# Optimization experiments

Hardware: AMD Instinct MI355X
Metric: run time of the kernel (lower is better)

Reference implementation:

```python
import jax, jax.numpy as jnp
import numpy as np

B = 2          # batch size
G = 96         # voxel grid extent per dim
RES = 0.04     # voxel resolution (meters)
STRIDE = 1.0   # sparse tensor stride
EPS = 1e-5     # batchnorm eps
C_SP = 32      # sparse feature channels
C_PF = 32      # pts_feat channels
H = 128        # hidden conv channels
NHYP = 7       # 2h+1, h=3


def setup_inputs():
    key = jax.random.key(0)
    ks = jax.random.split(key, 16)
    n = 150_000
    N = 2 * 9 * 56 * 56  # b * n_views * 56x56
    sparse_coords = jax.random.randint(ks[0], (n, 3), 0, G, dtype=jnp.int32)
    sparse_batch = jnp.sort(jax.random.randint(ks[1], (n,), 0, B, dtype=jnp.int32))
    sparse_feats = jax.random.normal(ks[2], (n, C_SP), jnp.float32)
    sparse_pts = sparse_coords.astype(jnp.float32) * RES  # world coordinates
    pts_depthmap_hyp = jax.random.uniform(ks[3], (N, NHYP, 3), jnp.float32) * (0.9 * G * RES)
    pts_feat = jax.random.normal(ks[4], (N, NHYP, C_PF), jnp.float32)
    pts_batch = jax.random.randint(ks[5], (N,), 0, B, dtype=jnp.int32)
    c_in = C_SP + C_PF
    def cw(k, o, i):
        return jax.random.normal(k, (o, i, 3), jnp.float32) * (1.0 / np.sqrt(i * 3))
    inp = dict(sparse_pts=sparse_pts, sparse_coords=sparse_coords, sparse_batch=sparse_batch,
               sparse_feats=sparse_feats, pts_depthmap_hyp=pts_depthmap_hyp,
               pts_feat=pts_feat, pts_batch=pts_batch)
    for li, (o, i, kk) in enumerate([(H, c_in, ks[6]), (H, H, ks[7]), (H, H, ks[8])], start=1):
        kw, km = jax.random.split(kk)
        inp[f'w{li}'] = cw(kw, o, i)
        inp[f'g{li}'] = jnp.ones((o,), jnp.float32)
        inp[f'b{li}'] = jnp.zeros((o,), jnp.float32)
        inp[f'm{li}'] = jax.random.normal(km, (o,), jnp.float32) * 0.1
        inp[f'v{li}'] = jnp.ones((o,), jnp.float32)
    inp['w4'] = cw(ks[9], 1, H)
    inp['bias4'] = jnp.zeros((1,), jnp.float32)
    return inp


def _trilinear_interp(coords, cbatch, feats, q, qb):
    """Sparse trilinear interpolation (MinkowskiInterpolation, stride 1).
    coords:(n,3) int voxel coords, cbatch:(n,), feats:(n,c), q:(M,3) float, qb:(M,).
    Missing corner voxels contribute zero."""
    n = coords.shape[0]
    keys = ((cbatch * G + coords[:, 0]) * G + coords[:, 1]) * G + coords[:, 2]
    order = jnp.argsort(keys)
    skeys = keys[order]
    sfeats = feats[order]
    fl = jnp.floor(q)
    frac = q - fl
    fli = fl.astype(jnp.int32)
    out = jnp.zeros((q.shape[0], feats.shape[1]), feats.dtype)
    for dx in (0, 1):
        for dy in (0, 1):
            for dz in (0, 1):
                c = fli + jnp.array([dx, dy, dz], jnp.int32)
                w = ((frac[:, 0] if dx else 1.0 - frac[:, 0]) *
                     (frac[:, 1] if dy else 1.0 - frac[:, 1]) *
                     (frac[:, 2] if dz else 1.0 - frac[:, 2]))
                qkey = ((qb * G + c[:, 0]) * G + c[:, 1]) * G + c[:, 2]
                idx = jnp.clip(jnp.searchsorted(skeys, qkey), 0, n - 1)
                hit = (skeys[idx] == qkey) & jnp.all((c >= 0) & (c < G), axis=1)
                out = out + jnp.where(hit, w, 0.0)[:, None] * sfeats[idx]
    return out


def _conv1d(x, w):  # x:(N,C,L), w:(O,C,3), pad 1
    return jax.lax.conv_general_dilated(x, w, (1,), [(1, 1)],
                                        dimension_numbers=('NCH', 'OIH', 'NCH'))


def _bn_relu(x, g, b, m, v):
    s = (g / jnp.sqrt(v + EPS))[None, :, None]
    return jax.nn.relu((x - m[None, :, None]) * s + b[None, :, None])


def reference(sparse_pts, sparse_coords, sparse_batch, sparse_feats,
              pts_depthmap_hyp, pts_feat, pts_batch,
              w1, g1, b1, m1, v1, w2, g2, b2, m2, v2, w3, g3, b3, m3, v3, w4, bias4):
    N, n_hyp = pts_depthmap_hyp.shape[0], pts_depthmap_hyp.shape[1]
    # scatter-min of point coordinates per batch element
    min_pts = jax.ops.segment_min(sparse_pts, sparse_batch, num_segments=B)  # (B,3)
    pts_idx = (pts_depthmap_hyp - min_pts[pts_batch][:, None, :]) / RES * STRIDE
    q = pts_idx.reshape(N * n_hyp, 3)
    qb = jnp.repeat(pts_batch, n_hyp)
    feats = _trilinear_interp(sparse_coords, sparse_batch, sparse_feats, q, qb)
    feats = feats.reshape(N, n_hyp, -1)
    x = jnp.concatenate([feats, pts_feat], axis=2).transpose(0, 2, 1)  # (N, C, n_hyp)
    h = _bn_relu(_conv1d(x, w1), g1, b1, m1, v1)
    h = _bn_relu(_conv1d(h, w2), g2, b2, m2, v2)
    h = _bn_relu(_conv1d(h, w3), g3, b3, m3, v3)
    logits = _conv1d(h, w4) + bias4[None, :, None]  # (N,1,n_hyp)
    return jax.nn.softmax(logits[:, 0, :], axis=1)  # (N, n_hyp)
```

## Files before the change

kernel.cpp:

```cpp
#include <hip/hip_runtime.h>

#define GG 96
#define NB 2
#define RESV 0.04f

constexpr int NG  = NB * GG * GG * GG;
constexpr int PT  = 16;
constexpr int NCOLS = PT * 8;
constexpr int XC  = NCOLS + 2;
constexpr int CS  = 136;

typedef _Float16 f16x8 __attribute__((ext_vector_type(8)));
typedef _Float16 f16x4 __attribute__((ext_vector_type(4)));
typedef _Float16 f16x2 __attribute__((ext_vector_type(2)));
typedef float    f32x4 __attribute__((ext_vector_type(4)));

__global__ void k_init(int4* __restrict__ grid4, int* __restrict__ minc) {
    int i = blockIdx.x * 256 + threadIdx.x;
    if (i < NG / 4) grid4[i] = make_int4(0x7fffffff, 0x7fffffff, 0x7fffffff, 0x7fffffff);
    if (i < 6)      minc[i] = 0x7fffffff;
}

__global__ void k_scatter(const int* __restrict__ coords, const int* __restrict__ sbatch,
                          int n, int* __restrict__ grid, int* __restrict__ minc) {
    __shared__ int lmin[6];
    int tid = threadIdx.x;
    if (tid < 6) lmin[tid] = 0x7fffffff;
    __syncthreads();
    int i = blockIdx.x * 256 + tid;
    if (i < n) {
        int cx = coords[3*i], cy = coords[3*i+1], cz = coords[3*i+2];
        int b = sbatch[i];
        atomicMin(&grid[((b*GG + cx)*GG + cy)*GG + cz], i);
        atomicMin(&lmin[b*3+0], cx);
        atomicMin(&lmin[b*3+1], cy);
        atomicMin(&lmin[b*3+2], cz);
    }
    __syncthreads();
    if (tid < 6) atomicMin(&minc[tid], lmin[tid]);
}

__global__ void k_wconv(const float* __restrict__ w1, const float* __restrict__ w2,
                        const float* __restrict__ w3,
                        const float* __restrict__ g1, const float* __restrict__ b1,
                        const float* __restrict__ m1, const float* __restrict__ v1,
                        const float* __restrict__ g2, const float* __restrict__ b2,
                        const float* __restrict__ m2, const float* __restrict__ v2,
                        const float* __restrict__ g3, const float* __restrict__ b3,
                        const float* __restrict__ m3, const float* __restrict__ v3,
                        _Float16* __restrict__ o1, _Float16* __restrict__ o2,
                        _Float16* __restrict__ o3, float* __restrict__ tvec) {
    int e = blockIdx.x * 256 + threadIdx.x;
    if (e < 24576) {
        int j = e & 7, lane = (e >> 3) & 63, t2 = e >> 9;
        int mt = t2 / 6, ks = t2 % 6;
        int row = mt * 16 + (lane & 15);
        int k = ks * 32 + ((lane >> 4) << 3) + j;
        int tap = k >> 6, c = k & 63;
        float s = g1[row] / sqrtf(v1[row] + 1e-5f);
        o1[e] = (_Float16)(w1[(row * 64 + c) * 3 + tap] * s);
    } else if (e < 122880) {
        int u = e - 24576;
        int layer = u / 49152;
        u %= 49152;
        int j = u & 7, lane = (u >> 3) & 63, t2 = u >> 9;
        int mt = t2 / 12, ks = t2 % 12;
        int row = mt * 16 + (lane & 15);
        int k = ks * 32 + ((lane >> 4) << 3) + j;
        int tap = k >> 7, c = k & 127;
        const float* w = layer ? w3 : w2;
        const float* g = layer ? g3 : g2;
        const float* v = layer ? v3 : v2;
        float s = g[row] / sqrtf(v[row] + 1e-5f);
        (layer ? o3 : o2)[u] = (_Float16)(w[(row * 128 + c) * 3 + tap] * s);
    } else if (e < 123264) {
        int i = e - 122880;
        int layer = i >> 7, ch = i & 127;
        const float* g = layer == 0 ? g1 : (layer == 1 ? g2 : g3);
        const float* b = layer == 0 ? b1 : (layer == 1 ? b2 : b3);
        const float* m = layer == 0 ? m1 : (layer == 1 ? m2 : m3);
        const float* v = layer == 0 ? v1 : (layer == 1 ? v2 : v3);
        float s = g[ch] / sqrtf(v[ch] + 1e-5f);
        tvec[i] = b[ch] - m[ch] * s;
    }
}

template<int CIN, int KS>
__device__ __forceinline__ void conv_layer(
    const _Float16* xin, const _Float16* __restrict__ wg,
    const float* tvl, _Float16* hout, int tid)
{
    const int wave = tid >> 6;
    const int lane = tid & 63;
    const int quad = lane >> 4;
    const int l15  = lane & 15;
    const int mp   = wave & 1;
    const int cb   = (wave >> 1) * 64;

    constexpr int PF = 3;
    f32x4 acc[4][4] = {};
    f16x8 Abuf[PF][4];
    f16x8 Bbuf[2][4];

    const _Float16* wbase = wg + (((size_t)(mp * 4) * KS) * 64 + lane) * 8;

    auto loadA = [&](int slot, int ks) {
#pragma unroll
        for (int m = 0; m < 4; ++m)
            Abuf[slot][m] = *(const f16x8*)(wbase + (size_t)(m * KS + ks) * 512);
    };
    auto loadB = [&](int slot, int ks) {
        const int k0   = ks * 32 + quad * 8;
        const int tap  = k0 / CIN;
        const int c    = k0 & (CIN - 1);
        const int boff = (cb + l15 + tap) * CS + c;
#pragma unroll
        for (int ct = 0; ct < 4; ++ct)
            Bbuf[slot][ct] = *(const f16x8*)(xin + boff + ct * 16 * CS);
    };

#pragma unroll
    for (int p = 0; p < PF; ++p) loadA(p, p);
    loadB(0, 0);

#pragma unroll
    for (int ks = 0; ks < KS; ++ks) {
        if (ks + 1 < KS) loadB((ks + 1) & 1, ks + 1);
#pragma unroll
        for (int ct = 0; ct < 4; ++ct)
#pragma unroll
            for (int m = 0; m < 4; ++m)
                acc[ct][m] = __builtin_amdgcn_mfma_f32_16x16x32_f16(
                    Abuf[ks % PF][m], Bbuf[ks & 1][ct], acc[ct][m], 0, 0, 0);
        if (ks + PF < KS) loadA(ks % PF, ks + PF);
    }

    if ((l15 & 7) != 7) {
#pragma unroll
        for (int ct = 0; ct < 4; ++ct) {
            const int outc = cb + ct * 16 + l15;
            _Float16* dst = hout + (outc + 1) * CS + mp * 64 + quad * 4;
#pragma unroll
            for (int m = 0; m < 4; ++m) {
                const int ch = mp * 64 + m * 16 + quad * 4;
                f32x4 tval = *(const f32x4*)(tvl + ch);
                f16x4 o;
#pragma unroll
                for (int i = 0; i < 4; ++i)
                    o[i] = (_Float16)fmaxf(acc[ct][m][i] + tval[i], 0.f);
                *(f16x4*)(dst + m * 16) = o;
            }
        }
    }
}

__global__ __launch_bounds__(256, 2) void k_main(
    const float* __restrict__ pdh, const float* __restrict__ ptsfeat,
    const int* __restrict__ pts_batch, const float* __restrict__ sfeats,
    const int* __restrict__ grid, const int* __restrict__ minc,
    const _Float16* __restrict__ w16_1, const _Float16* __restrict__ w16_2,
    const _Float16* __restrict__ w16_3, const float* __restrict__ tvec,
    const float* __restrict__ w4, const float* __restrict__ bias4,
    float* __restrict__ out, int N, int n_sp)
{
    __shared__ __align__(16) _Float16 hA[XC * CS];
    __shared__ __align__(16) _Float16 hB[XC * CS];
    __shared__ __align__(16) float    tv[384];
    __shared__ __align__(16) _Float16 w4h[384];
    __shared__ float lg[NCOLS];

    const int tid = threadIdx.x;
    const int p0  = blockIdx.x * PT;

    for (int e = tid; e < 384; e += 256) {
        tv[e]  = tvec[e];
        w4h[e] = (_Float16)w4[(e & 127) * 3 + (e >> 7)];
    }
    for (int idx = tid; idx < 18 * (CS / 2); idx += 256) {
        int cidx = idx / (CS / 2), off = idx % (CS / 2);
        int u = (cidx < 17) ? cidx * 8 : 129;
        ((int*)hA)[u * (CS / 2) + off] = 0;
        ((int*)hB)[u * (CS / 2) + off] = 0;
    }

    if (tid < 224) {
        int q = tid >> 1, part = tid & 1;
        int pl = q / 7, j = q - pl * 7;
        int pg = p0 + pl;
        if (pg < N) {
            const f32x4* pf = (const f32x4*)(ptsfeat + ((size_t)pg * 7 + j) * 32 + part * 16);
            f32x4 pf0 = __builtin_nontemporal_load(pf + 0);
            f32x4 pf1 = __builtin_nontemporal_load(pf + 1);
            f32x4 pf2 = __builtin_nontemporal_load(pf + 2);
            f32x4 pf3 = __builtin_nontemporal_load(pf + 3);
            const float* pd = pdh + ((size_t)pg * 7 + j) * 3;
            float px = pd[0], py = pd[1], pz = pd[2];
            int b = pts_batch[pg];
            int mA0 = minc[0], mA1 = minc[1], mA2 = minc[2];
            int mB0 = minc[3], mB1 = minc[4], mB2 = minc[5];
            int m0 = b ? mB0 : mA0;
            int m1 = b ? mB1 : mA1;
            int m2 = b ? mB2 : mA2;
            float qx = (px - (float)m0 * RESV) / RESV;
            float qy = (py - (float)m1 * RESV) / RESV;
            float qz = (pz - (float)m2 * RESV) / RESV;
            float flx = floorf(qx), fly = floorf(qy), flz = floorf(qz);
            float fx = qx - flx, fy = qy - fly, fz = qz - flz;
            int ix0 = (int)flx, iy0 = (int)fly, iz0 = (int)flz;
            const int gbase = b * (GG * GG * GG);

            int   si[8];
            float wc[8];
#pragma unroll
            for (int c = 0; c < 8; ++c) {
                int dx = c >> 2, dy = (c >> 1) & 1, dz = c & 1;
                int cx = ix0 + dx, cy = iy0 + dy, cz = iz0 + dz;
                bool ok = ((unsigned)cx < GG) & ((unsigned)cy < GG) & ((unsigned)cz < GG);
                int cell = gbase + (cx * GG + cy) * GG + cz;
                wc[c] = ok ? (dx ? fx : 1.f - fx) * (dy ? fy : 1.f - fy)
                             * (dz ? fz : 1.f - fz)
                           : 0.f;
                si[c] = grid[ok ? cell : 0];
            }
            const f32x4* fb = (const f32x4*)sfeats;
            const f32x4* fpc[8];
            float w8[8];
#pragma unroll
            for (int c = 0; c < 8; ++c) {
                bool hit = si[c] < n_sp;
                w8[c]  = hit ? wc[c] : 0.f;
                fpc[c] = fb + (size_t)(hit ? si[c] : 0) * 8 + part * 4;
            }
            float acc[16];
#pragma unroll
            for (int k2 = 0; k2 < 16; ++k2) acc[k2] = 0.f;
#pragma unroll
            for (int c = 0; c < 8; ++c) {
                f32x4 f0 = fpc[c][0], f1 = fpc[c][1], f2 = fpc[c][2], f3 = fpc[c][3];
                float w = w8[c];
#pragma unroll
                for (int k2 = 0; k2 < 4; ++k2) {
                    acc[k2]      += w * f0[k2];
                    acc[4 + k2]  += w * f1[k2];
                    acc[8 + k2]  += w * f2[k2];
                    acc[12 + k2] += w * f3[k2];
                }
            }
            int u = pl * 8 + 1 + j;
            _Float16* xp = hA + u * CS + part * 16;
            f16x8 h0, h1;
#pragma unroll
            for (int k2 = 0; k2 < 8; ++k2) { h0[k2] = (_Float16)acc[k2]; h1[k2] = (_Float16)acc[8 + k2]; }
            *(f16x8*)xp = h0;
            *(f16x8*)(xp + 8) = h1;
            f16x8 p0v, p1v;
#pragma unroll
            for (int k2 = 0; k2 < 4; ++k2) {
                p0v[k2]     = (_Float16)pf0[k2];
                p0v[4 + k2] = (_Float16)pf1[k2];
                p1v[k2]     = (_Float16)pf2[k2];
                p1v[4 + k2] = (_Float16)pf3[k2];
            }
            *(f16x8*)(hA + u * CS + 32 + part * 16) = p0v;
            *(f16x8*)(hA + u * CS + 40 + part * 16) = p1v;
        }
    }
    __syncthreads();

    conv_layer<64,  6>(hA, w16_1, tv,       hB, tid);
    __syncthreads();
    conv_layer<128, 12>(hB, w16_2, tv + 128, hA, tid);
    __syncthreads();
    conv_layer<128, 12>(hA, w16_3, tv + 256, hB, tid);
    __syncthreads();

    {
        int col = tid >> 1, part = tid & 1;
        float sum = 0.f;
        if ((col & 7) != 7) {
#pragma unroll
            for (int t = 0; t < 3; ++t) {
                const _Float16* hp = hB + (col + t) * CS;
                const _Float16* wr = w4h + t * 128;
#pragma unroll
                for (int c8 = 0; c8 < 8; ++c8) {
                    int chunk = 2 * c8 + part;
                    f16x8 h8 = *(const f16x8*)(hp + chunk * 8);
                    f16x8 w8 = *(const f16x8*)(wr + chunk * 8);
#pragma unroll
                    for (int p = 0; p < 4; ++p) {
                        f16x2 hv = { h8[2*p], h8[2*p+1] };
                        f16x2 wv = { w8[2*p], w8[2*p+1] };
#if __has_builtin(__builtin_amdgcn_fdot2)
                        sum = __builtin_amdgcn_fdot2(hv, wv, sum, false);
#else
                        sum += (float)hv[0]*(float)wv[0] + (float)hv[1]*(float)wv[1];
#endif
                    }
                }
            }
        }
        sum += __shfl_xor(sum, 1);
        if (part == 0 && (col & 7) != 7) lg[col] = sum + bias4[0];
    }
    __syncthreads();

    if (tid < PT) {
        int pg = p0 + tid;
        if (pg < N) {
            float l0[7];
            float mx = -1e30f;
#pragma unroll
            for (int j = 0; j < 7; ++j) { l0[j] = lg[tid * 8 + j]; mx = fmaxf(mx, l0[j]); }
            float s = 0.f;
#pragma unroll
            for (int j = 0; j < 7; ++j) { l0[j] = __expf(l0[j] - mx); s += l0[j]; }
            float inv = 1.f / s;
#pragma unroll
            for (int j = 0; j < 7; ++j) out[(size_t)pg * 7 + j] = l0[j] * inv;
        }
    }
}

extern "C" void kernel_launch(void* const* d_in, const int* in_sizes, int n_in,
                              void* d_out, int out_size, void* d_ws, size_t ws_size,
                              hipStream_t stream) {
    const int*   sparse_coords = (const int*)d_in[1];
    const int*   sparse_batch  = (const int*)d_in[2];
    const float* sparse_feats  = (const float*)d_in[3];
    const float* pdh           = (const float*)d_in[4];
    const float* ptsfeat       = (const float*)d_in[5];
    const int*   pts_batch     = (const int*)d_in[6];
    const float* w1 = (const float*)d_in[7];
    const float* g1 = (const float*)d_in[8],  *b1 = (const float*)d_in[9];
    const float* m1 = (const float*)d_in[10], *v1 = (const float*)d_in[11];
    const float* w2 = (const float*)d_in[12];
    const float* g2 = (const float*)d_in[13], *b2 = (const float*)d_in[14];
    const float* m2 = (const float*)d_in[15], *v2 = (const float*)d_in[16];
    const float* w3 = (const float*)d_in[17];
    const float* g3 = (const float*)d_in[18], *b3 = (const float*)d_in[19];
    const float* m3 = (const float*)d_in[20], *v3 = (const float*)d_in[21];
    const float* w4 = (const float*)d_in[22];
    const float* bias4 = (const float*)d_in[23];

    const int n_sp = in_sizes[2];
    const int N    = in_sizes[6];

    int* grid = (int*)d_ws;
    int* minc = grid + NG;
    _Float16* w16_1 = (_Float16*)((char*)d_ws + (size_t)(NG + 6) * 4 + 8);
    _Float16* w16_2 = w16_1 + 128 * 192;
    _Float16* w16_3 = w16_2 + 128 * 384;
    float*    tvec  = (float*)(w16_3 + 128 * 384);

    k_init<<<(NG / 4 + 255) / 256, 256, 0, stream>>>((int4*)grid, minc);
    k_scatter<<<(n_sp + 255) / 256, 256, 0, stream>>>(sparse_coords, sparse_batch,
                                                      n_sp, grid, minc);
    k_wconv<<<482, 256, 0, stream>>>(w1, w2, w3,
                                     g1, b1, m1, v1, g2, b2, m2, v2, g3, b3, m3, v3,
                                     w16_1, w16_2, w16_3, tvec);
    k_main<<<(N + PT - 1) / PT, 256, 0, stream>>>(
        pdh, ptsfeat, pts_batch, sparse_feats, grid, minc,
        w16_1, w16_2, w16_3, tvec, w4, bias4, (float*)d_out, N, n_sp);
}
```

Measured before the change: 158.1 us.

## Make main kernel persistent and software-pipeline the gather across conv layers

The main kernel becomes persistent: a grid of at most 512 blocks loops over point tiles. The gather and interpolation for the next tile is split into stages (global loads, grid lookups, feature accumulation, LDS write) placed between the three conv layers of the current tile, so memory latency overlaps MFMA work. The shared-memory logit buffer and its extra barrier are replaced by a wave-shuffle softmax. In exchange, register pressure rises from the live prefetch state, and load balance depends on the fixed grid size.

```diff
diff --git a/kernel.cpp b/kernel.cpp
--- a/kernel.cpp
+++ b/kernel.cpp
@@ -167,10 +167,10 @@
     __shared__ __align__(16) _Float16 hB[XC * CS];
     __shared__ __align__(16) float    tv[384];
     __shared__ __align__(16) _Float16 w4h[384];
-    __shared__ float lg[NCOLS];
 
     const int tid = threadIdx.x;
-    const int p0  = blockIdx.x * PT;
+    const int G   = gridDim.x;
+    const int ntiles = (N + PT - 1) / PT;
 
     for (int e = tid; e < 384; e += 256) {
         tv[e]  = tvec[e];
@@ -178,39 +178,63 @@
     }
     for (int idx = tid; idx < 18 * (CS / 2); idx += 256) {
         int cidx = idx / (CS / 2), off = idx % (CS / 2);
-        int u = (cidx < 17) ? cidx * 8 : 129;
-        ((int*)hA)[u * (CS / 2) + off] = 0;
-        ((int*)hB)[u * (CS / 2) + off] = 0;
-    }
-
-    if (tid < 224) {
-        int q = tid >> 1, part = tid & 1;
-        int pl = q / 7, j = q - pl * 7;
-        int pg = p0 + pl;
-        if (pg < N) {
-            const f32x4* pf = (const f32x4*)(ptsfeat + ((size_t)pg * 7 + j) * 32 + part * 16);
-            f32x4 pf0 = __builtin_nontemporal_load(pf + 0);
-            f32x4 pf1 = __builtin_nontemporal_load(pf + 1);
-            f32x4 pf2 = __builtin_nontemporal_load(pf + 2);
-            f32x4 pf3 = __builtin_nontemporal_load(pf + 3);
-            const float* pd = pdh + ((size_t)pg * 7 + j) * 3;
-            float px = pd[0], py = pd[1], pz = pd[2];
-            int b = pts_batch[pg];
-            int mA0 = minc[0], mA1 = minc[1], mA2 = minc[2];
-            int mB0 = minc[3], mB1 = minc[4], mB2 = minc[5];
-            int m0 = b ? mB0 : mA0;
-            int m1 = b ? mB1 : mA1;
-            int m2 = b ? mB2 : mA2;
+        int u2 = (cidx < 17) ? cidx * 8 : 129;
+        ((int*)hA)[u2 * (CS / 2) + off] = 0;
+        ((int*)hB)[u2 * (CS / 2) + off] = 0;
+    }
+
+    const bool ip  = tid < 224;
+    const int  q   = tid >> 1, part = tid & 1;
+    const int  pl  = q / 7, jj = q - pl * 7;
+    const int  u   = pl * 8 + 1 + jj;
+    const int  mA0 = minc[0], mA1 = minc[1], mA2 = minc[2];
+    const int  mB0 = minc[3], mB1 = minc[4], mB2 = minc[5];
+    const float b4 = bias4[0];
+
+    f32x4 pf0, pf1, pf2, pf3;
+    float px = 0.f, py = 0.f, pz = 0.f;
+    int   bsel = 0;
+    int   si[8];
+    float wc[8];
+    f16x8 p0v, p1v, h0, h1;
+    bool  nv = false;
+
+    auto stage1 = [&](int tt) {
+        nv = false;
+        if (ip && tt < ntiles) {
+            int pg = tt * PT + pl;
+            if (pg < N) {
+                nv = true;
+                const f32x4* pf = (const f32x4*)(ptsfeat + ((size_t)pg * 7 + jj) * 32 + part * 16);
+                pf0 = __builtin_nontemporal_load(pf + 0);
+                pf1 = __builtin_nontemporal_load(pf + 1);
+                pf2 = __builtin_nontemporal_load(pf + 2);
+                pf3 = __builtin_nontemporal_load(pf + 3);
+                const float* pd = pdh + ((size_t)pg * 7 + jj) * 3;
+                px = pd[0]; py = pd[1]; pz = pd[2];
+                bsel = pts_batch[pg];
+            }
+        }
+    };
+    auto stage2 = [&]() {
+        if (nv) {
+#pragma unroll
+            for (int k2 = 0; k2 < 4; ++k2) {
+                p0v[k2]     = (_Float16)pf0[k2];
+                p0v[4 + k2] = (_Float16)pf1[k2];
+                p1v[k2]     = (_Float16)pf2[k2];
+                p1v[4 + k2] = (_Float16)pf3[k2];
+            }
+            int m0 = bsel ? mB0 : mA0;
+            int m1 = bsel ? mB1 : mA1;
+            int m2 = bsel ? mB2 : mA2;
             float qx = (px - (float)m0 * RESV) / RESV;
             float qy = (py - (float)m1 * RESV) / RESV;
             float qz = (pz - (float)m2 * RESV) / RESV;
             float flx = floorf(qx), fly = floorf(qy), flz = floorf(qz);
             float fx = qx - flx, fy = qy - fly, fz = qz - flz;
             int ix0 = (int)flx, iy0 = (int)fly, iz0 = (int)flz;
-            const int gbase = b * (GG * GG * GG);
-
-            int   si[8];
-            float wc[8];
+            const int gbase = bsel * (GG * GG * GG);
 #pragma unroll
             for (int c = 0; c < 8; ++c) {
                 int dx = c >> 2, dy = (c >> 1) & 1, dz = c & 1;
@@ -222,6 +246,10 @@
                            : 0.f;
                 si[c] = grid[ok ? cell : 0];
             }
+        }
+    };
+    auto stage3 = [&]() {
+        if (nv) {
             const f32x4* fb = (const f32x4*)sfeats;
             const f32x4* fpc[8];
             float w8[8];
@@ -246,79 +274,82 @@
                     acc[12 + k2] += w * f3[k2];
                 }
             }
-            int u = pl * 8 + 1 + j;
+#pragma unroll
+            for (int k2 = 0; k2 < 8; ++k2) {
+                h0[k2] = (_Float16)acc[k2];
+                h1[k2] = (_Float16)acc[8 + k2];
+            }
+        }
+    };
+    auto writeR = [&]() {
+        if (nv) {
             _Float16* xp = hA + u * CS + part * 16;
-            f16x8 h0, h1;
-#pragma unroll
-            for (int k2 = 0; k2 < 8; ++k2) { h0[k2] = (_Float16)acc[k2]; h1[k2] = (_Float16)acc[8 + k2]; }
-            *(f16x8*)xp = h0;
+            *(f16x8*)xp       = h0;
             *(f16x8*)(xp + 8) = h1;
-            f16x8 p0v, p1v;
-#pragma unroll
-            for (int k2 = 0; k2 < 4; ++k2) {
-                p0v[k2]     = (_Float16)pf0[k2];
-                p0v[4 + k2] = (_Float16)pf1[k2];
-                p1v[k2]     = (_Float16)pf2[k2];
-                p1v[4 + k2] = (_Float16)pf3[k2];
-            }
             *(f16x8*)(hA + u * CS + 32 + part * 16) = p0v;
             *(f16x8*)(hA + u * CS + 40 + part * 16) = p1v;
         }
-    }
+    };
+
+    int tile = blockIdx.x;
+    stage1(tile); stage2(); stage3(); writeR();
     __syncthreads();
 
-    conv_layer<64,  6>(hA, w16_1, tv,       hB, tid);
-    __syncthreads();
-    conv_layer<128, 12>(hB, w16_2, tv + 128, hA, tid);
-    __syncthreads();
-    conv_layer<128, 12>(hA, w16_3, tv + 256, hB, tid);
-    __syncthreads();
-
-    {
-        int col = tid >> 1, part = tid & 1;
-        float sum = 0.f;
-        if ((col & 7) != 7) {
-#pragma unroll
-            for (int t = 0; t < 3; ++t) {
-                const _Float16* hp = hB + (col + t) * CS;
-                const _Float16* wr = w4h + t * 128;
-#pragma unroll
-                for (int c8 = 0; c8 < 8; ++c8) {
-                    int chunk = 2 * c8 + part;
-                    f16x8 h8 = *(const f16x8*)(hp + chunk * 8);
-                    f16x8 w8 = *(const f16x8*)(wr + chunk * 8);
-#pragma unroll
-                    for (int p = 0; p < 4; ++p) {
-                        f16x2 hv = { h8[2*p], h8[2*p+1] };
-                        f16x2 wv = { w8[2*p], w8[2*p+1] };
+    for (; tile < ntiles; tile += G) {
+        stage1(tile + G);
+        conv_layer<64,  6>(hA, w16_1, tv,       hB, tid);
+        __syncthreads();
+        stage2();
+        conv_layer<128, 12>(hB, w16_2, tv + 128, hA, tid);
+        __syncthreads();
+        stage3();
+        conv_layer<128, 12>(hA, w16_3, tv + 256, hB, tid);
+        __syncthreads();
+        writeR();
+        {
+            int col = tid >> 1, p4 = tid & 1;
+            float sum = 0.f;
+            if ((col & 7) != 7) {
+#pragma unroll
+                for (int t = 0; t < 3; ++t) {
+                    const _Float16* hp = hB + (col + t) * CS;
+                    const _Float16* wr = w4h + t * 128;
+#pragma unroll
+                    for (int c8 = 0; c8 < 8; ++c8) {
+                        int chunk = 2 * c8 + p4;
+                        f16x8 h8 = *(const f16x8*)(hp + chunk * 8);
+                        f16x8 w8 = *(const f16x8*)(wr + chunk * 8);
+#pragma unroll
+                        for (int p = 0; p < 4; ++p) {
+                            f16x2 hv = { h8[2*p], h8[2*p+1] };
+                            f16x2 wv = { w8[2*p], w8[2*p+1] };
 #if __has_builtin(__builtin_amdgcn_fdot2)
-                        sum = __builtin_amdgcn_fdot2(hv, wv, sum, false);
+                            sum = __builtin_amdgcn_fdot2(hv, wv, sum, false);
 #else
-                        sum += (float)hv[0]*(float)wv[0] + (float)hv[1]*(float)wv[1];
+                            sum += (float)hv[0]*(float)wv[0] + (float)hv[1]*(float)wv[1];
 #endif
+                        }
                     }
                 }
             }
-        }
-        sum += __shfl_xor(sum, 1);
-        if (part == 0 && (col & 7) != 7) lg[col] = sum + bias4[0];
-    }
-    __syncthreads();
-
-    if (tid < PT) {
-        int pg = p0 + tid;
-        if (pg < N) {
-            float l0[7];
-            float mx = -1e30f;
-#pragma unroll
-            for (int j = 0; j < 7; ++j) { l0[j] = lg[tid * 8 + j]; mx = fmaxf(mx, l0[j]); }
-            float s = 0.f;
-#pragma unroll
-            for (int j = 0; j < 7; ++j) { l0[j] = __expf(l0[j] - mx); s += l0[j]; }
-            float inv = 1.f / s;
-#pragma unroll
-            for (int j = 0; j < 7; ++j) out[(size_t)pg * 7 + j] = l0[j] * inv;
-        }
+            sum += __shfl_xor(sum, 1);
+            float logit = sum + b4;
+            bool  dead  = (col & 7) == 7;
+            float v = dead ? -1e30f : logit;
+            v = fmaxf(v, __shfl_xor(v, 2));
+            v = fmaxf(v, __shfl_xor(v, 4));
+            v = fmaxf(v, __shfl_xor(v, 8));
+            float e = (!dead && p4 == 0) ? __expf(logit - v) : 0.f;
+            float es = e;
+            es += __shfl_xor(es, 2);
+            es += __shfl_xor(es, 4);
+            es += __shfl_xor(es, 8);
+            if (p4 == 0 && !dead) {
+                int pgt = tile * PT + (col >> 3);
+                if (pgt < N) out[(size_t)pgt * 7 + (col & 7)] = e / es;
+            }
+        }
+        __syncthreads();
     }
 }
 
@@ -359,7 +390,9 @@
     k_wconv<<<482, 256, 0, stream>>>(w1, w2, w3,
                                      g1, b1, m1, v1, g2, b2, m2, v2, g3, b3, m3, v3,
                                      w16_1, w16_2, w16_3, tvec);
-    k_main<<<(N + PT - 1) / PT, 256, 0, stream>>>(
+    const int ntiles = (N + PT - 1) / PT;
+    const int gsz = ntiles < 512 ? ntiles : 512;
+    k_main<<<gsz, 256, 0, stream>>>(
         pdh, ptsfeat, pts_batch, sparse_feats, grid, minc,
         w16_1, w16_2, w16_3, tvec, w4, bias4, (float*)d_out, N, n_sp);
 }
```

After: 436.5 us. 2.76x slower.

## Split trilinear interpolation into separate kernel and shuffle-based softmax

Applied to the files above, without the earlier changes.

Moves the gather-heavy trilinear interpolation and pts_feat conversion out of the conv kernel into a standalone high-occupancy kernel that writes fp16 inputs to a global workspace buffer. The main kernel then just copies these inputs into LDS, so its latency-bound gathers no longer stall the MFMA-heavy block. The softmax now uses warp shuffles instead of an LDS round trip and an extra barrier. The cost is an extra global write and read of about 56k*7*64 fp16 values, plus one more kernel launch.

```diff
diff --git a/kernel.cpp b/kernel.cpp
--- a/kernel.cpp
+++ b/kernel.cpp
@@ -85,6 +85,92 @@
     }
 }
 
+__global__ __launch_bounds__(256, 4) void k_interp(
+    const float* __restrict__ pdh, const float* __restrict__ ptsfeat,
+    const int* __restrict__ pts_batch, const float* __restrict__ sfeats,
+    const int* __restrict__ grid, const int* __restrict__ minc,
+    _Float16* __restrict__ Xg, int NQ, int n_sp)
+{
+    int t = blockIdx.x * 256 + threadIdx.x;
+    int gq = t >> 1, part = t & 1;
+    if (gq >= NQ) return;
+    int pg = gq / 7;
+
+    const f32x4* pf = (const f32x4*)(ptsfeat + (size_t)gq * 32 + part * 16);
+    f32x4 pf0 = __builtin_nontemporal_load(pf + 0);
+    f32x4 pf1 = __builtin_nontemporal_load(pf + 1);
+    f32x4 pf2 = __builtin_nontemporal_load(pf + 2);
+    f32x4 pf3 = __builtin_nontemporal_load(pf + 3);
+    const float* pd = pdh + (size_t)gq * 3;
+    float px = pd[0], py = pd[1], pz = pd[2];
+    int b = pts_batch[pg];
+    int mA0 = minc[0], mA1 = minc[1], mA2 = minc[2];
+    int mB0 = minc[3], mB1 = minc[4], mB2 = minc[5];
+    int m0 = b ? mB0 : mA0;
+    int m1 = b ? mB1 : mA1;
+    int m2 = b ? mB2 : mA2;
+    float qx = (px - (float)m0 * RESV) / RESV;
+    float qy = (py - (float)m1 * RESV) / RESV;
+    float qz = (pz - (float)m2 * RESV) / RESV;
+    float flx = floorf(qx), fly = floorf(qy), flz = floorf(qz);
+    float fx = qx - flx, fy = qy - fly, fz = qz - flz;
+    int ix0 = (int)flx, iy0 = (int)fly, iz0 = (int)flz;
+    const int gbase = b * (GG * GG * GG);
+
+    int   si[8];
+    float wc[8];
+#pragma unroll
+    for (int c = 0; c < 8; ++c) {
+        int dx = c >> 2, dy = (c >> 1) & 1, dz = c & 1;
+        int cx = ix0 + dx, cy = iy0 + dy, cz = iz0 + dz;
+        bool ok = ((unsigned)cx < GG) & ((unsigned)cy < GG) & ((unsigned)cz < GG);
+        int cell = gbase + (cx * GG + cy) * GG + cz;
+        wc[c] = ok ? (dx ? fx : 1.f - fx) * (dy ? fy : 1.f - fy)
+                     * (dz ? fz : 1.f - fz)
+                   : 0.f;
+        si[c] = grid[ok ? cell : 0];
+    }
+    const f32x4* fb = (const f32x4*)sfeats;
+    const f32x4* fpc[8];
+    float w8[8];
+#pragma unroll
+    for (int c = 0; c < 8; ++c) {
+        bool hit = si[c] < n_sp;
+        w8[c]  = hit ? wc[c] : 0.f;
+        fpc[c] = fb + (size_t)(hit ? si[c] : 0) * 8 + part * 4;
+    }
+    float acc[16];
+#pragma unroll
+    for (int k2 = 0; k2 < 16; ++k2) acc[k2] = 0.f;
+#pragma unroll
+    for (int c = 0; c < 8; ++c) {
+        f32x4 f0 = fpc[c][0], f1 = fpc[c][1], f2 = fpc[c][2], f3 = fpc[c][3];
+        float w = w8[c];
+#pragma unroll
+        for (int k2 = 0; k2 < 4; ++k2) {
+            acc[k2]      += w * f0[k2];
+            acc[4 + k2]  += w * f1[k2];
+            acc[8 + k2]  += w * f2[k2];
+            acc[12 + k2] += w * f3[k2];
+        }
+    }
+    f16x8 h0, h1, p0v, p1v;
+#pragma unroll
+    for (int k2 = 0; k2 < 8; ++k2) { h0[k2] = (_Float16)acc[k2]; h1[k2] = (_Float16)acc[8 + k2]; }
+#pragma unroll
+    for (int k2 = 0; k2 < 4; ++k2) {
+        p0v[k2]     = (_Float16)pf0[k2];
+        p0v[4 + k2] = (_Float16)pf1[k2];
+        p1v[k2]     = (_Float16)pf2[k2];
+        p1v[4 + k2] = (_Float16)pf3[k2];
+    }
+    _Float16* xp = Xg + (size_t)gq * 64;
+    *(f16x8*)(xp + part * 16)          = h0;
+    *(f16x8*)(xp + part * 16 + 8)      = h1;
+    *(f16x8*)(xp + 32 + part * 16)     = p0v;
+    *(f16x8*)(xp + 32 + part * 16 + 8) = p1v;
+}
+
 template<int CIN, int KS>
 __device__ __forceinline__ void conv_layer(
     const _Float16* xin, const _Float16* __restrict__ wg,
@@ -155,19 +241,16 @@
 }
 
 __global__ __launch_bounds__(256, 2) void k_main(
-    const float* __restrict__ pdh, const float* __restrict__ ptsfeat,
-    const int* __restrict__ pts_batch, const float* __restrict__ sfeats,
-    const int* __restrict__ grid, const int* __restrict__ minc,
+    const _Float16* __restrict__ Xg,
     const _Float16* __restrict__ w16_1, const _Float16* __restrict__ w16_2,
     const _Float16* __restrict__ w16_3, const float* __restrict__ tvec,
     const float* __restrict__ w4, const float* __restrict__ bias4,
-    float* __restrict__ out, int N, int n_sp)
+    float* __restrict__ out, int N)
 {
     __shared__ __align__(16) _Float16 hA[XC * CS];
     __shared__ __align__(16) _Float16 hB[XC * CS];
     __shared__ __align__(16) float    tv[384];
     __shared__ __align__(16) _Float16 w4h[384];
-    __shared__ float lg[NCOLS];
 
     const int tid = threadIdx.x;
     const int p0  = blockIdx.x * PT;
@@ -184,85 +267,18 @@
     }
 
     if (tid < 224) {
-        int q = tid >> 1, part = tid & 1;
-        int pl = q / 7, j = q - pl * 7;
+        int qi = tid >> 1, part = tid & 1;
+        int pl = qi / 7, j = qi - pl * 7;
         int pg = p0 + pl;
         if (pg < N) {
-            const f32x4* pf = (const f32x4*)(ptsfeat + ((size_t)pg * 7 + j) * 32 + part * 16);
-            f32x4 pf0 = __builtin_nontemporal_load(pf + 0);
-            f32x4 pf1 = __builtin_nontemporal_load(pf + 1);
-            f32x4 pf2 = __builtin_nontemporal_load(pf + 2);
-            f32x4 pf3 = __builtin_nontemporal_load(pf + 3);
-            const float* pd = pdh + ((size_t)pg * 7 + j) * 3;
-            float px = pd[0], py = pd[1], pz = pd[2];
-            int b = pts_batch[pg];
-            int mA0 = minc[0], mA1 = minc[1], mA2 = minc[2];
-            int mB0 = minc[3], mB1 = minc[4], mB2 = minc[5];
-            int m0 = b ? mB0 : mA0;
-            int m1 = b ? mB1 : mA1;
-            int m2 = b ? mB2 : mA2;
-            float qx = (px - (float)m0 * RESV) / RESV;
-            float qy = (py - (float)m1 * RESV) / RESV;
-            float qz = (pz - (float)m2 * RESV) / RESV;
-            float flx = floorf(qx), fly = floorf(qy), flz = floorf(qz);
-            float fx = qx - flx, fy = qy - fly, fz = qz - flz;
-            int ix0 = (int)flx, iy0 = (int)fly, iz0 = (int)flz;
-            const int gbase = b * (GG * GG * GG);
-
-            int   si[8];
-            float wc[8];
-#pragma unroll
-            for (int c = 0; c < 8; ++c) {
-                int dx = c >> 2, dy = (c >> 1) & 1, dz = c & 1;
-                int cx = ix0 + dx, cy = iy0 + dy, cz = iz0 + dz;
-                bool ok = ((unsigned)cx < GG) & ((unsigned)cy < GG) & ((unsigned)cz < GG);
-                int cell = gbase + (cx * GG + cy) * GG + cz;
-                wc[c] = ok ? (dx ? fx : 1.f - fx) * (dy ? fy : 1.f - fy)
-                             * (dz ? fz : 1.f - fz)
-                           : 0.f;
-                si[c] = grid[ok ? cell : 0];
-            }
-            const f32x4* fb = (const f32x4*)sfeats;
-            const f32x4* fpc[8];
-            float w8[8];
-#pragma unroll
-            for (int c = 0; c < 8; ++c) {
-                bool hit = si[c] < n_sp;
-                w8[c]  = hit ? wc[c] : 0.f;
-                fpc[c] = fb + (size_t)(hit ? si[c] : 0) * 8 + part * 4;
-            }
-            float acc[16];
-#pragma unroll
-            for (int k2 = 0; k2 < 16; ++k2) acc[k2] = 0.f;
-#pragma unroll
-            for (int c = 0; c < 8; ++c) {
-                f32x4 f0 = fpc[c][0], f1 = fpc[c][1], f2 = fpc[c][2], f3 = fpc[c][3];
-                float w = w8[c];
-#pragma unroll
-                for (int k2 = 0; k2 < 4; ++k2) {
-                    acc[k2]      += w * f0[k2];
-                    acc[4 + k2]  += w * f1[k2];
-                    acc[8 + k2]  += w * f2[k2];
-                    acc[12 + k2] += w * f3[k2];
-                }
-            }
-            int u = pl * 8 + 1 + j;
-            _Float16* xp = hA + u * CS + part * 16;
-            f16x8 h0, h1;
-#pragma unroll
-            for (int k2 = 0; k2 < 8; ++k2) { h0[k2] = (_Float16)acc[k2]; h1[k2] = (_Float16)acc[8 + k2]; }
-            *(f16x8*)xp = h0;
-            *(f16x8*)(xp + 8) = h1;
-            f16x8 p0v, p1v;
-#pragma unroll
-            for (int k2 = 0; k2 < 4; ++k2) {
-                p0v[k2]     = (_Float16)pf0[k2];
-                p0v[4 + k2] = (_Float16)pf1[k2];
-                p1v[k2]     = (_Float16)pf2[k2];
-                p1v[4 + k2] = (_Float16)pf3[k2];
-            }
-            *(f16x8*)(hA + u * CS + 32 + part * 16) = p0v;
-            *(f16x8*)(hA + u * CS + 40 + part * 16) = p1v;
+            const f16x8* src = (const f16x8*)(Xg + ((size_t)pg * 7 + j) * 64);
+            f16x8 a = src[2 * part], b = src[2 * part + 1];
+            f16x8 c = src[4 + 2 * part], d = src[4 + 2 * part + 1];
+            _Float16* xp = hA + (pl * 8 + 1 + j) * CS;
+            *(f16x8*)(xp + part * 16)          = a;
+            *(f16x8*)(xp + part * 16 + 8)      = b;
+            *(f16x8*)(xp + 32 + part * 16)     = c;
+            *(f16x8*)(xp + 32 + part * 16 + 8) = d;
         }
     }
     __syncthreads();
@@ -275,7 +291,7 @@
     __syncthreads();
 
     {
-        int col = tid >> 1, part = tid & 1;
+        int col = tid >> 1, p4 = tid & 1;
         float sum = 0.f;
         if ((col & 7) != 7) {
 #pragma unroll
@@ -284,7 +300,7 @@
                 const _Float16* wr = w4h + t * 128;
 #pragma unroll
                 for (int c8 = 0; c8 < 8; ++c8) {
-                    int chunk = 2 * c8 + part;
+                    int chunk = 2 * c8 + p4;
                     f16x8 h8 = *(const f16x8*)(hp + chunk * 8);
                     f16x8 w8 = *(const f16x8*)(wr + chunk * 8);
 #pragma unroll
@@ -301,23 +317,20 @@
             }
         }
         sum += __shfl_xor(sum, 1);
-        if (part == 0 && (col & 7) != 7) lg[col] = sum + bias4[0];
-    }
-    __syncthreads();
-
-    if (tid < PT) {
-        int pg = p0 + tid;
-        if (pg < N) {
-            float l0[7];
-            float mx = -1e30f;
-#pragma unroll
-            for (int j = 0; j < 7; ++j) { l0[j] = lg[tid * 8 + j]; mx = fmaxf(mx, l0[j]); }
-            float s = 0.f;
-#pragma unroll
-            for (int j = 0; j < 7; ++j) { l0[j] = __expf(l0[j] - mx); s += l0[j]; }
-            float inv = 1.f / s;
-#pragma unroll
-            for (int j = 0; j < 7; ++j) out[(size_t)pg * 7 + j] = l0[j] * inv;
+        float logit = sum + bias4[0];
+        bool  dead  = (col & 7) == 7;
+        float v = dead ? -1e30f : logit;
+        v = fmaxf(v, __shfl_xor(v, 2));
+        v = fmaxf(v, __shfl_xor(v, 4));
+        v = fmaxf(v, __shfl_xor(v, 8));
+        float e = (!dead && p4 == 0) ? __expf(logit - v) : 0.f;
+        float es = e;
+        es += __shfl_xor(es, 2);
+        es += __shfl_xor(es, 4);
+        es += __shfl_xor(es, 8);
+        if (p4 == 0 && !dead) {
+            int pgt = p0 + (col >> 3);
+            if (pgt < N) out[(size_t)pgt * 7 + (col & 7)] = e / es;
         }
     }
 }
@@ -345,6 +358,7 @@
 
     const int n_sp = in_sizes[2];
     const int N    = in_sizes[6];
+    const int NQ   = N * 7;
 
     int* grid = (int*)d_ws;
     int* minc = grid + NG;
@@ -352,6 +366,7 @@
     _Float16* w16_2 = w16_1 + 128 * 192;
     _Float16* w16_3 = w16_2 + 128 * 384;
     float*    tvec  = (float*)(w16_3 + 128 * 384);
+    _Float16* Xg    = (_Float16*)(tvec + 384);
 
     k_init<<<(NG / 4 + 255) / 256, 256, 0, stream>>>((int4*)grid, minc);
     k_scatter<<<(n_sp + 255) / 256, 256, 0, stream>>>(sparse_coords, sparse_batch,
@@ -359,7 +374,8 @@
     k_wconv<<<482, 256, 0, stream>>>(w1, w2, w3,
                                      g1, b1, m1, v1, g2, b2, m2, v2, g3, b3, m3, v3,
                                      w16_1, w16_2, w16_3, tvec);
+    k_interp<<<(2 * NQ + 255) / 256, 256, 0, stream>>>(
+        pdh, ptsfeat, pts_batch, sparse_feats, grid, minc, Xg, NQ, n_sp);
     k_main<<<(N + PT - 1) / PT, 256, 0, stream>>>(
-        pdh, ptsfeat, pts_batch, sparse_feats, grid, minc,
-        w16_1, w16_2, w16_3, tvec, w4, bias4, (float*)d_out, N, n_sp);
-}
+        Xg, w16_1, w16_2, w16_3, tvec, w4, bias4, (float*)d_out, N);
+}
```

After: 184.3 us. 16.6% more time.
